# Kernel optimization log

Hardware: AMD Instinct MI355X
Metric: run time of the kernel (lower is better)

Reference implementation:

```python
import jax, jax.numpy as jnp
import numpy as np

B, S, D, DH = 4, 2048, 1024, 64


def setup_inputs() -> dict:
    key = jax.random.key(0)
    ks = jax.random.split(key, 7)
    x = jax.random.normal(ks[0], (B, S, D), dtype=jnp.float32)
    def w(k):
        return jax.random.normal(k, (D, DH), dtype=jnp.float32) / np.sqrt(D).astype(np.float32)
    return {
        'x': x,
        'w_q_u': w(ks[1]), 'w_k_u': w(ks[2]), 'w_v_u': w(ks[3]),
        'w_q_c': w(ks[4]), 'w_k_c': w(ks[5]), 'w_v_c': w(ks[6]),
    }


def reference(x, w_q_u, w_k_u, w_v_u, w_q_c, w_k_c, w_v_c):
    b, n, _ = x.shape
    scale = w_q_u.shape[-1] ** -0.5
    # projections (LinearNoBias -> plain matmul)
    Q_u = x @ w_q_u
    K_u = x @ w_k_u
    V_u = x @ w_v_u
    Q_c = x @ w_q_c
    K_c = x @ w_k_c
    V_c = x @ w_v_c

    i = jnp.arange(n)
    causal = i[:, None] >= i[None, :]        # True where j <= i (binary causal / keep for S_c)
    lookahead = i[:, None] < i[None, :]      # True where j > i (allowed in sigmoid term)

    # term1: [b, n, n], zeroed above the diagonal via binary causal mask
    term1 = jnp.einsum('bid,bjd->bij', Q_c, V_u) * scale * causal.astype(x.dtype)

    # sigmoid gate: lookahead mask adds -inf on/below the diagonal -> sigmoid = 0 there
    logits_u = jnp.einsum('bid,bjd->bij', Q_u, K_u) * scale
    sigmoid_term = jax.nn.sigmoid(jnp.where(lookahead, logits_u, -jnp.inf))

    # nested n^3 matmul: S_u[b,i,k] = sum_j term1[b,i,j] * sigmoid_term[b,k,j]
    S_u = jnp.einsum('bij,bkj->bik', term1, sigmoid_term)

    S_c = jnp.where(causal, jnp.einsum('bid,bjd->bij', Q_c, K_c) * scale, -jnp.inf)

    attn = jax.nn.softmax(S_c - jax.nn.silu(S_u), axis=-1)
    return jnp.einsum('bij,bjd->bid', attn, V_c)
```

## Files before the change

### kernel.cpp

```cpp
#include <hip/hip_runtime.h>
#include <hip/hip_bf16.h>

typedef short bf16x8 __attribute__((ext_vector_type(8)));
typedef float f32x4  __attribute__((ext_vector_type(4)));
typedef _Float16 f16x4 __attribute__((ext_vector_type(4)));
typedef _Float16 f16x8 __attribute__((ext_vector_type(8)));

#define MFMA16(a,b,c)  __builtin_amdgcn_mfma_f32_16x16x32_bf16((a),(b),(c),0,0,0)
#define MFMAF16(a,b,c) __builtin_amdgcn_mfma_f32_16x16x32_f16((a),(b),(c),0,0,0)

#define GLDS16(g,l) __builtin_amdgcn_global_load_lds( \
    (const __attribute__((address_space(1))) void*)(g), \
    (__attribute__((address_space(3))) void*)(l), 16, 0, 0)

__device__ __forceinline__ short f2bf(float f){
  union { float f; unsigned u; } v; v.f = f;
  unsigned r = v.u + 0x7fffu + ((v.u >> 16) & 1u);
  return (short)(r >> 16);
}
__device__ __forceinline__ float bf2f(short h){
  union { unsigned u; float f; } v; v.u = ((unsigned)(unsigned short)h) << 16;
  return v.f;
}
__device__ __forceinline__ void split8v(f32x4 a, f32x4 b, bf16x8& h, bf16x8& l){
  float t[8] = {a[0],a[1],a[2],a[3],b[0],b[1],b[2],b[3]};
  #pragma unroll
  for (int e = 0; e < 8; ++e){
    short hs = f2bf(t[e]);
    h[e] = hs;
    l[e] = f2bf(t[e] - bf2f(hs));
  }
}

__global__ void k_wt(const float* w0, const float* w1, const float* w2,
                     const float* w3, const float* w4, const float* w5,
                     unsigned short* __restrict__ wth, unsigned short* __restrict__ wtl){
  int p = blockIdx.y;
  const float* wp = p==0?w0:p==1?w1:p==2?w2:p==3?w3:p==4?w4:w5;
  int idx = blockIdx.x*256 + threadIdx.x;
  int n = idx >> 10, k = idx & 1023;
  float v = wp[k*64 + n];
  short hs = f2bf(v);
  wth[(size_t)p*65536 + n*1024 + k] = (unsigned short)hs;
  wtl[(size_t)p*65536 + n*1024 + k] = (unsigned short)f2bf(v - bf2f(hs));
}

__global__ void k_xsplit(const float* __restrict__ x,
                         unsigned short* __restrict__ xh, unsigned short* __restrict__ xl){
  size_t i = ((size_t)blockIdx.x*256 + threadIdx.x)*8;
  f32x4 a = *(const f32x4*)(x + i);
  f32x4 b = *(const f32x4*)(x + i + 4);
  bf16x8 h, l;
  split8v(a, b, h, l);
  *(bf16x8*)(xh + i) = h;
  *(bf16x8*)(xl + i) = l;
}

__global__ __launch_bounds__(256) void k_proj(
    const unsigned short* __restrict__ xh, const unsigned short* __restrict__ xl,
    const unsigned short* __restrict__ wth, const unsigned short* __restrict__ wtl,
    float* __restrict__ proj,
    unsigned short* __restrict__ projh, unsigned short* __restrict__ projl){
  __shared__ __align__(16) char sm[49152];
  int blk = blockIdx.x;
  int rb = blk/6, p = blk - rb*6;
  int tid = threadIdx.x, w = tid >> 6, lane = tid & 63;
  int lm = lane & 15, quad = lane >> 4;
  int srow = lane >> 3, scg = (lane & 7) ^ srow;
  const char* xhg = (const char*)xh;
  const char* xlg = (const char*)xl;
  const char* wthp = (const char*)wth + (size_t)p*131072;
  const char* wtlp = (const char*)wtl + (size_t)p*131072;
  int wm = w*32;
  f32x4 acc[2][4] = {};
  for (int k0 = 0; k0 < 1024; k0 += 64){
    __syncthreads();
    size_t cb = (size_t)k0*2 + scg*16;
    #pragma unroll
    for (int i2 = 0; i2 < 4; ++i2){
      int i = w*4 + i2;
      size_t g = (size_t)(rb*128 + i*8 + srow)*2048 + cb;
      GLDS16(xhg + g, sm +         i*1024);
      GLDS16(xlg + g, sm + 16384 + i*1024);
    }
    #pragma unroll
    for (int i2 = 0; i2 < 2; ++i2){
      int i = w*2 + i2;
      size_t g = (size_t)(i*8 + srow)*2048 + cb;
      GLDS16(wthp + g, sm + 32768 + i*1024);
      GLDS16(wtlp + g, sm + 40960 + i*1024);
    }
    __syncthreads();
    #pragma unroll
    for (int ks = 0; ks < 2; ++ks){
      bf16x8 bh[4], bl[4];
      #pragma unroll
      for (int n = 0; n < 4; ++n){
        int r = n*16 + lm;
        int off = r*128 + (((ks*4+quad) ^ (r&7))*16);
        bh[n] = *(const bf16x8*)(sm + 32768 + off);
        bl[n] = *(const bf16x8*)(sm + 40960 + off);
      }
      #pragma unroll
      for (int m = 0; m < 2; ++m){
        int r = wm + m*16 + lm;
        int off = r*128 + (((ks*4+quad) ^ (r&7))*16);
        bf16x8 ah = *(const bf16x8*)(sm + off);
        bf16x8 al = *(const bf16x8*)(sm + 16384 + off);
        #pragma unroll
        for (int n = 0; n < 4; ++n){
          acc[m][n] = MFMA16(ah, bh[n], acc[m][n]);
          acc[m][n] = MFMA16(ah, bl[n], acc[m][n]);
          acc[m][n] = MFMA16(al, bh[n], acc[m][n]);
        }
      }
    }
  }
  if (p == 5){
    float* op = proj + (size_t)p*524288;
    #pragma unroll
    for (int m = 0; m < 2; ++m)
      #pragma unroll
      for (int n = 0; n < 4; ++n)
        #pragma unroll
        for (int e = 0; e < 4; ++e){
          int r = rb*128 + wm + m*16 + quad*4 + e;
          op[(size_t)r*64 + n*16 + lm] = acc[m][n][e];
        }
  } else {
    unsigned short* oph = projh + (size_t)p*524288;
    unsigned short* opl = projl + (size_t)p*524288;
    #pragma unroll
    for (int m = 0; m < 2; ++m)
      #pragma unroll
      for (int n = 0; n < 4; ++n)
        #pragma unroll
        for (int e = 0; e < 4; ++e){
          int r = rb*128 + wm + m*16 + quad*4 + e;
          float f = acc[m][n][e];
          short hs = f2bf(f);
          oph[(size_t)r*64 + n*16 + lm] = (unsigned short)hs;
          opl[(size_t)r*64 + n*16 + lm] = (unsigned short)f2bf(f - bf2f(hs));
        }
  }
}

__global__ void k_vct(const float* __restrict__ proj, _Float16* __restrict__ vct){
  __shared__ float T[64][65];
  int b = blockIdx.y, st = blockIdx.x;
  int tid = threadIdx.x;
  const float* vc = proj + 5*524288 + (size_t)b*131072;
  int sloc = tid >> 2, cp = (tid & 3)*16;
  #pragma unroll
  for (int j = 0; j < 4; ++j){
    f32x4 v = *(const f32x4*)(vc + (size_t)(st*64 + sloc)*64 + cp + j*4);
    #pragma unroll
    for (int e = 0; e < 4; ++e) T[sloc][cp + j*4 + e] = v[e];
  }
  __syncthreads();
  int d = tid >> 2, sp = (tid & 3)*16;
  f16x8 h0, h1;
  #pragma unroll
  for (int j = 0; j < 8; ++j) h0[j] = (_Float16)T[sp + j][d];
  #pragma unroll
  for (int j = 0; j < 8; ++j) h1[j] = (_Float16)T[sp + 8 + j][d];
  size_t o = (size_t)b*131072 + (size_t)d*2048 + st*64 + sp;
  *(f16x8*)(vct + o) = h0; *(f16x8*)(vct + o + 8) = h1;
}

__global__ __launch_bounds__(256,2) void k_p2(
    const unsigned short* __restrict__ ph, const unsigned short* __restrict__ pl,
    _Float16* __restrict__ t1, _Float16* __restrict__ sg){
  __shared__ __align__(16) char sm[65536];
  int b = blockIdx.y;
  int t = blockIdx.x;
  bool isSig = t >= 136;
  if (isSig) t -= 136;
  int a = 0, bb = 0;
  #pragma unroll 1
  for (int aa = 0; aa < 16; ++aa){
    int c = isSig ? (16 - aa) : (aa + 1);
    if (t < c){ a = aa; bb = isSig ? (aa + t) : t; break; }
    t -= c;
  }
  int pa = isSig ? 0 : 3;
  int pb = isSig ? 1 : 2;
  const char* Ahg = (const char*)ph + (size_t)pa*1048576;
  const char* Alg = (const char*)pl + (size_t)pa*1048576;
  const char* Bhg = (const char*)ph + (size_t)pb*1048576;
  const char* Blg = (const char*)pl + (size_t)pb*1048576;
  int tid = threadIdx.x, w = tid >> 6, lane = tid & 63;
  int lm = lane & 15, quad = lane >> 4;
  int srow = lane >> 3, scg = (lane & 7) ^ srow;
  int wm = (w & 1)*64, wn = (w >> 1)*64;
  #pragma unroll
  for (int i2 = 0; i2 < 4; ++i2){
    int i = w*4 + i2;
    int rl = i*8 + srow;
    size_t ga = (size_t)(b*2048 + a*128  + rl)*128 + scg*16;
    size_t gb = (size_t)(b*2048 + bb*128 + rl)*128 + scg*16;
    GLDS16(Ahg + ga, sm +         i*1024);
    GLDS16(Alg + ga, sm + 16384 + i*1024);
    GLDS16(Bhg + gb, sm + 32768 + i*1024);
    GLDS16(Blg + gb, sm + 49152 + i*1024);
  }
  __syncthreads();
  f32x4 acc[4][4] = {};
  #pragma unroll
  for (int ks = 0; ks < 2; ++ks){
    bf16x8 bh[4], bl[4];
    #pragma unroll
    for (int n = 0; n < 4; ++n){
      int r = wn + n*16 + lm;
      int off = r*128 + (((ks*4+quad) ^ (r&7))*16);
      bh[n] = *(const bf16x8*)(sm + 32768 + off);
      bl[n] = *(const bf16x8*)(sm + 49152 + off);
    }
    #pragma unroll
    for (int m = 0; m < 4; ++m){
      int r = wm + m*16 + lm;
      int off = r*128 + (((ks*4+quad) ^ (r&7))*16);
      bf16x8 ah = *(const bf16x8*)(sm + off);
      bf16x8 al = *(const bf16x8*)(sm + 16384 + off);
      #pragma unroll
      for (int n = 0; n < 4; ++n){
        acc[m][n] = MFMA16(ah, bh[n], acc[m][n]);
        acc[m][n] = MFMA16(ah, bl[n], acc[m][n]);
        acc[m][n] = MFMA16(al, bh[n], acc[m][n]);
      }
    }
  }
  __syncthreads();
  _Float16* Tt = (_Float16*)sm;
  #pragma unroll
  for (int m = 0; m < 4; ++m){
    #pragma unroll
    for (int n = 0; n < 4; ++n){
      #pragma unroll
      for (int e = 0; e < 4; ++e){
        int il = wm + m*16 + quad*4 + e;
        int jl = wn + n*16 + lm;
        int gi = a*128 + il, gj = bb*128 + jl;
        float v = acc[m][n][e] * 0.125f;
        float outv;
        if (!isSig) outv = (gj <= gi) ? v : 0.0f;
        else        outv = (gj >  gi) ? (1.0f/(1.0f + __expf(-v))) : 0.0f;
        Tt[il*128 + jl] = (_Float16)outv;
      }
    }
  }
  __syncthreads();
  _Float16* outp = (isSig ? sg : t1) + (size_t)b*4194304;
  #pragma unroll
  for (int r = 0; r < 8; ++r){
    int lrow = w*32 + r*4 + (lane >> 4);
    int c16 = lane & 15;
    f32x4 vv = *(const f32x4*)(sm + lrow*256 + c16*16);
    *(f32x4*)((char*)(outp + (size_t)(a*128 + lrow)*2048 + bb*128) + c16*16) = vv;
  }
}

__global__ __launch_bounds__(256,2) void k_p3(
    const unsigned short* __restrict__ ph, const unsigned short* __restrict__ pl,
    const _Float16* __restrict__ t1, const _Float16* __restrict__ sg,
    _Float16* __restrict__ lg){
  __shared__ __align__(16) char sm[32768];
  int b = blockIdx.y;
  int v = blockIdx.x, I = 0, K = 0;
  #pragma unroll 1
  for (int d = 15; d >= 0; --d){
    int nd = 16 - d;
    if (v < nd){ I = d + v; K = v; break; }
    v -= nd;
  }
  int tid = threadIdx.x, w = tid >> 6, lane = tid & 63;
  int lm = lane & 15, quad = lane >> 4;
  size_t mat = (size_t)b * 4194304;
  const char* Ag = (const char*)(t1 + mat);
  const char* Bg = (const char*)(sg + mat);
  int srow = lane >> 3, scg = (lane & 7) ^ srow;
  int wm = (w & 1)*64, wn = (w >> 1)*64;
  f32x4 su[4][4] = {};
  for (int j64 = 2*K; j64 <= 2*I + 1; ++j64){
    __syncthreads();
    size_t colb = (size_t)j64*128 + scg*16;
    #pragma unroll
    for (int i2 = 0; i2 < 4; ++i2){
      int i = w*4 + i2;
      int rl = i*8 + srow;
      GLDS16(Ag + (size_t)(I*128 + rl)*4096 + colb, sm +         i*1024);
      GLDS16(Bg + (size_t)(K*128 + rl)*4096 + colb, sm + 16384 + i*1024);
    }
    __syncthreads();
    #pragma unroll
    for (int ks = 0; ks < 2; ++ks){
      f16x8 bf[4];
      #pragma unroll
      for (int n = 0; n < 4; ++n){
        int r = wn + n*16 + lm;
        bf[n] = *(const f16x8*)(sm + 16384 + r*128 + (((ks*4+quad) ^ (r&7))*16));
      }
      #pragma unroll
      for (int m = 0; m < 4; ++m){
        int r = wm + m*16 + lm;
        f16x8 af = *(const f16x8*)(sm + r*128 + (((ks*4+quad) ^ (r&7))*16));
        #pragma unroll
        for (int n = 0; n < 4; ++n)
          su[m][n] = MFMAF16(af, bf[n], su[m][n]);
      }
    }
  }
  const char* Qh = (const char*)ph + (size_t)3*1048576;
  const char* Ql = (const char*)pl + (size_t)3*1048576;
  const char* Kh = (const char*)ph + (size_t)4*1048576;
  const char* Kl = (const char*)pl + (size_t)4*1048576;
  f32x4 sc[4][4] = {};
  #pragma unroll
  for (int ks = 0; ks < 2; ++ks){
    bf16x8 kh[4], kl[4];
    #pragma unroll
    for (int n = 0; n < 4; ++n){
      size_t off = (size_t)(b*2048 + K*128 + wn + n*16 + lm)*128 + (ks*32 + quad*8)*2;
      kh[n] = *(const bf16x8*)(Kh + off);
      kl[n] = *(const bf16x8*)(Kl + off);
    }
    #pragma unroll
    for (int m = 0; m < 4; ++m){
      size_t off = (size_t)(b*2048 + I*128 + wm + m*16 + lm)*128 + (ks*32 + quad*8)*2;
      bf16x8 ah = *(const bf16x8*)(Qh + off);
      bf16x8 al = *(const bf16x8*)(Ql + off);
      #pragma unroll
      for (int n = 0; n < 4; ++n){
        sc[m][n] = MFMA16(ah, kh[n], sc[m][n]);
        sc[m][n] = MFMA16(ah, kl[n], sc[m][n]);
        sc[m][n] = MFMA16(al, kh[n], sc[m][n]);
      }
    }
  }
  __syncthreads();
  _Float16* Tt = (_Float16*)sm;
  #pragma unroll
  for (int m = 0; m < 4; ++m){
    #pragma unroll
    for (int n = 0; n < 4; ++n){
      #pragma unroll
      for (int e = 0; e < 4; ++e){
        int il = wm + m*16 + quad*4 + e;
        int jl = wn + n*16 + lm;
        float xv = su[m][n][e];
        float sgm = 1.0f/(1.0f + __expf(-xv));
        Tt[il*128 + jl] = (_Float16)(sc[m][n][e]*0.125f - xv*sgm);
      }
    }
  }
  __syncthreads();
  _Float16* lgb = lg + mat;
  #pragma unroll
  for (int r = 0; r < 8; ++r){
    int lrow = w*32 + r*4 + (lane >> 4);
    int c16 = lane & 15;
    f32x4 vv = *(const f32x4*)(sm + lrow*256 + c16*16);
    *(f32x4*)((char*)(lgb + (size_t)(I*128 + lrow)*2048 + K*128) + c16*16) = vv;
  }
}

__global__ __launch_bounds__(256) void k_p4a(const _Float16* __restrict__ lg,
    float* __restrict__ mrow, float* __restrict__ zrow){
  int b = blockIdx.y;
  int wid = blockIdx.x*4 + (threadIdx.x >> 6);
  int row = 2047 - wid;
  int lane = threadIdx.x & 63;
  const _Float16* lr = lg + (size_t)b*4194304u + (size_t)row*2048;
  float m_r = -1.0e30f, s_r = 0.0f;
  int nch = (row >> 9) + 1;
  for (int it = 0; it < nch; ++it){
    int base = it*512 + lane*8;
    if (base <= row){
      f16x8 vv = *(const f16x8*)(lr + base);
      float xs[8]; float mc = -1.0e30f;
      #pragma unroll
      for (int e = 0; e < 8; ++e){
        xs[e] = (base + e <= row) ? (float)vv[e] : -1.0e30f;
        mc = fmaxf(mc, xs[e]);
      }
      float mm = fmaxf(m_r, mc);
      float s = 0.0f;
      #pragma unroll
      for (int e = 0; e < 8; ++e)
        if (xs[e] > -1.0e29f) s += __expf(xs[e] - mm);
      s_r = (m_r > -1.0e29f ? s_r*__expf(m_r - mm) : 0.0f) + s;
      m_r = mm;
    }
  }
  #pragma unroll
  for (int off = 32; off; off >>= 1){
    float mo = __shfl_xor(m_r, off);
    float so = __shfl_xor(s_r, off);
    float mm = fmaxf(m_r, mo);
    float s = 0.0f;
    if (m_r > -1.0e29f) s += s_r*__expf(m_r - mm);
    if (mo  > -1.0e29f) s += so *__expf(mo  - mm);
    m_r = mm; s_r = s;
  }
  if (lane == 0){
    mrow[b*2048 + row] = m_r;
    zrow[b*2048 + row] = s_r;
  }
}

__global__ __launch_bounds__(256) void k_p4b(const _Float16* __restrict__ lg,
    const _Float16* __restrict__ vct,
    const float* __restrict__ mrow, const float* __restrict__ zrow,
    float* __restrict__ out){
  __shared__ __align__(16) float Ot[4][16][64];
  __shared__ __align__(16) _Float16 Ls[4][16][64];
  int b = blockIdx.y;
  int band = 127 - blockIdx.x;
  int r0 = band*16;
  int tid = threadIdx.x, w = tid >> 6, lane = tid & 63;
  int lm = lane & 15, quad = lane >> 4;
  const _Float16* lgb = lg + (size_t)b*4194304u;
  const _Float16* vb = vct + (size_t)b*131072;
  int arow = r0 + lm;
  float mv = mrow[b*2048 + arow];
  int nkt = ((r0 + 15) >> 6) + 1;
  int fc = (r0 + 1) >> 6;
  int sr = lane >> 2, sc4 = (lane & 3)*16;
  f32x4 acc[4] = {};
  for (int kt = w; kt < nkt; kt += 4){
    const _Float16* src = lgb + (size_t)(r0 + sr)*2048 + kt*64 + sc4;
    *(f16x8*)&Ls[w][sr][sc4]     = *(const f16x8*)src;
    *(f16x8*)&Ls[w][sr][sc4 + 8] = *(const f16x8*)(src + 8);
    bool full = kt < fc;
    #pragma unroll
    for (int ks = 0; ks < 2; ++ks){
      int jbase = kt*64 + ks*32 + quad*8;
      f16x8 Lv = *(const f16x8*)&Ls[w][lm][ks*32 + quad*8];
      f16x8 af;
      #pragma unroll
      for (int e = 0; e < 8; ++e){
        float p = __expf((float)Lv[e] - mv);
        if (!full && (jbase + e > arow)) p = 0.0f;
        af[e] = (_Float16)p;
      }
      #pragma unroll
      for (int n = 0; n < 4; ++n){
        f16x8 bv = *(const f16x8*)(vb + (size_t)(n*16 + lm)*2048 + jbase);
        acc[n] = MFMAF16(af, bv, acc[n]);
      }
    }
  }
  #pragma unroll
  for (int n = 0; n < 4; ++n)
    #pragma unroll
    for (int e = 0; e < 4; ++e)
      Ot[w][quad*4 + e][n*16 + lm] = acc[n][e];
  __syncthreads();
  int row = tid >> 4, c4 = (tid & 15)*4;
  f32x4 s = *(const f32x4*)&Ot[0][row][c4];
  #pragma unroll
  for (int ww = 1; ww < 4; ++ww){
    f32x4 t = *(const f32x4*)&Ot[ww][row][c4];
    s[0]+=t[0]; s[1]+=t[1]; s[2]+=t[2]; s[3]+=t[3];
  }
  float z = zrow[b*2048 + r0 + row];
  f32x4 o = { s[0]/z, s[1]/z, s[2]/z, s[3]/z };
  *(f32x4*)(out + ((size_t)b*2048 + r0 + row)*64 + c4) = o;
}

static const size_t OFF_PROJ  = 0;
static const size_t OFF_WTH   = 12582912;
static const size_t OFF_WTL   = 13369344;
static const size_t OFF_PROJH = 14155776;
static const size_t OFF_PROJL = 20447232;
static const size_t OFF_VCT   = 26738688;
static const size_t OFF_T1    = 27787264;
static const size_t OFF_SG    = 61341696;
static const size_t OFF_LG    = 94896128;
static const size_t OFF_XH    = 128450560;
static const size_t OFF_XL    = 145227776;

extern "C" void kernel_launch(void* const* d_in, const int* in_sizes, int n_in,
                              void* d_out, int out_size, void* d_ws, size_t ws_size,
                              hipStream_t stream){
  (void)in_sizes; (void)n_in; (void)out_size; (void)ws_size;
  const float* x = (const float*)d_in[0];
  char* ws = (char*)d_ws;
  float*          proj  = (float*)(ws + OFF_PROJ);
  unsigned short* wth   = (unsigned short*)(ws + OFF_WTH);
  unsigned short* wtl   = (unsigned short*)(ws + OFF_WTL);
  unsigned short* projh = (unsigned short*)(ws + OFF_PROJH);
  unsigned short* projl = (unsigned short*)(ws + OFF_PROJL);
  _Float16*       vct   = (_Float16*)(ws + OFF_VCT);
  _Float16*       t1    = (_Float16*)(ws + OFF_T1);
  _Float16*       sg    = (_Float16*)(ws + OFF_SG);
  _Float16*       lg    = (_Float16*)(ws + OFF_LG);
  unsigned short* xh    = (unsigned short*)(ws + OFF_XH);
  unsigned short* xl    = (unsigned short*)(ws + OFF_XL);
  float*          mbuf  = (float*)(ws + OFF_WTH);
  float*          zbuf  = (float*)(ws + OFF_WTL);

  k_wt    <<<dim3(256,6),  256, 0, stream>>>((const float*)d_in[1], (const float*)d_in[2],
                                             (const float*)d_in[3], (const float*)d_in[4],
                                             (const float*)d_in[5], (const float*)d_in[6], wth, wtl);
  k_xsplit<<<dim3(4096),   256, 0, stream>>>(x, xh, xl);
  k_proj  <<<dim3(384),    256, 0, stream>>>(xh, xl, wth, wtl, proj, projh, projl);
  k_vct   <<<dim3(32,4),   256, 0, stream>>>(proj, vct);
  k_p2    <<<dim3(272,4),  256, 0, stream>>>(projh, projl, t1, sg);
  k_p3    <<<dim3(136,4),  256, 0, stream>>>(projh, projl, t1, sg, lg);
  k_p4a   <<<dim3(512,4),  256, 0, stream>>>(lg, mbuf, zbuf);
  k_p4b   <<<dim3(128,4),  256, 0, stream>>>(lg, vct, mbuf, zbuf, (float*)d_out);
}
```

Baseline: 227.9 us.

## Retile projection, double-buffer p3 loads, fuse softmax stats into PV kernel

Three separate changes. The projection kernel now tiles 64 rows by two weight matrices per block instead of 128 rows by one, so x is reloaded fewer times across outputs. The nested-matmul kernel double-buffers its LDS tiles (64KB), overlapping global-to-LDS loads with MFMA work. The separate row max/sum kernel is merged into the PV kernel: each block loads its 16-row band of logits into LDS once, computes max and sum there, then reuses it for the weighted sum, removing one launch and one read of the logits. The cost is larger LDS per block, which may limit occupancy, and extra syncthreads.

```diff
diff --git a/kernel.cpp b/kernel.cpp
--- a/kernel.cpp
+++ b/kernel.cpp
@@ -3,7 +3,6 @@
 
 typedef short bf16x8 __attribute__((ext_vector_type(8)));
 typedef float f32x4  __attribute__((ext_vector_type(4)));
-typedef _Float16 f16x4 __attribute__((ext_vector_type(4)));
 typedef _Float16 f16x8 __attribute__((ext_vector_type(8)));
 
 #define MFMA16(a,b,c)  __builtin_amdgcn_mfma_f32_16x16x32_bf16((a),(b),(c),0,0,0)
@@ -63,85 +62,80 @@
     unsigned short* __restrict__ projh, unsigned short* __restrict__ projl){
   __shared__ __align__(16) char sm[49152];
   int blk = blockIdx.x;
-  int rb = blk/6, p = blk - rb*6;
+  int rb = blk/3, pg = blk - rb*3;
   int tid = threadIdx.x, w = tid >> 6, lane = tid & 63;
   int lm = lane & 15, quad = lane >> 4;
   int srow = lane >> 3, scg = (lane & 7) ^ srow;
   const char* xhg = (const char*)xh;
   const char* xlg = (const char*)xl;
-  const char* wthp = (const char*)wth + (size_t)p*131072;
-  const char* wtlp = (const char*)wtl + (size_t)p*131072;
-  int wm = w*32;
+  const char* w0h = (const char*)wth + (size_t)(pg*2  )*131072;
+  const char* w0l = (const char*)wtl + (size_t)(pg*2  )*131072;
+  const char* w1h = (const char*)wth + (size_t)(pg*2+1)*131072;
+  const char* w1l = (const char*)wtl + (size_t)(pg*2+1)*131072;
   f32x4 acc[2][4] = {};
   for (int k0 = 0; k0 < 1024; k0 += 64){
     __syncthreads();
     size_t cb = (size_t)k0*2 + scg*16;
     #pragma unroll
-    for (int i2 = 0; i2 < 4; ++i2){
-      int i = w*4 + i2;
-      size_t g = (size_t)(rb*128 + i*8 + srow)*2048 + cb;
-      GLDS16(xhg + g, sm +         i*1024);
-      GLDS16(xlg + g, sm + 16384 + i*1024);
-    }
-    #pragma unroll
     for (int i2 = 0; i2 < 2; ++i2){
       int i = w*2 + i2;
-      size_t g = (size_t)(i*8 + srow)*2048 + cb;
-      GLDS16(wthp + g, sm + 32768 + i*1024);
-      GLDS16(wtlp + g, sm + 40960 + i*1024);
+      size_t gx = (size_t)(rb*64 + i*8 + srow)*2048 + cb;
+      size_t gw = (size_t)(i*8 + srow)*2048 + cb;
+      GLDS16(xhg + gx, sm +         i*1024);
+      GLDS16(xlg + gx, sm +  8192 + i*1024);
+      GLDS16(w0h + gw, sm + 16384 + i*1024);
+      GLDS16(w0l + gw, sm + 24576 + i*1024);
+      GLDS16(w1h + gw, sm + 32768 + i*1024);
+      GLDS16(w1l + gw, sm + 40960 + i*1024);
     }
     __syncthreads();
     #pragma unroll
     for (int ks = 0; ks < 2; ++ks){
-      bf16x8 bh[4], bl[4];
-      #pragma unroll
-      for (int n = 0; n < 4; ++n){
-        int r = n*16 + lm;
-        int off = r*128 + (((ks*4+quad) ^ (r&7))*16);
-        bh[n] = *(const bf16x8*)(sm + 32768 + off);
-        bl[n] = *(const bf16x8*)(sm + 40960 + off);
-      }
-      #pragma unroll
-      for (int m = 0; m < 2; ++m){
-        int r = wm + m*16 + lm;
-        int off = r*128 + (((ks*4+quad) ^ (r&7))*16);
-        bf16x8 ah = *(const bf16x8*)(sm + off);
-        bf16x8 al = *(const bf16x8*)(sm + 16384 + off);
+      int ra = w*16 + lm;
+      int offa = ra*128 + (((ks*4+quad) ^ (ra&7))*16);
+      bf16x8 ah = *(const bf16x8*)(sm + offa);
+      bf16x8 al = *(const bf16x8*)(sm + 8192 + offa);
+      #pragma unroll
+      for (int sub = 0; sub < 2; ++sub){
         #pragma unroll
         for (int n = 0; n < 4; ++n){
-          acc[m][n] = MFMA16(ah, bh[n], acc[m][n]);
-          acc[m][n] = MFMA16(ah, bl[n], acc[m][n]);
-          acc[m][n] = MFMA16(al, bh[n], acc[m][n]);
+          int r = n*16 + lm;
+          int off = r*128 + (((ks*4+quad) ^ (r&7))*16);
+          bf16x8 bh = *(const bf16x8*)(sm + 16384 + sub*16384 + off);
+          bf16x8 bl = *(const bf16x8*)(sm + 24576 + sub*16384 + off);
+          acc[sub][n] = MFMA16(ah, bh, acc[sub][n]);
+          acc[sub][n] = MFMA16(ah, bl, acc[sub][n]);
+          acc[sub][n] = MFMA16(al, bh, acc[sub][n]);
         }
       }
     }
   }
-  if (p == 5){
-    float* op = proj + (size_t)p*524288;
-    #pragma unroll
-    for (int m = 0; m < 2; ++m)
+  #pragma unroll
+  for (int sub = 0; sub < 2; ++sub){
+    int p = pg*2 + sub;
+    if (p == 5){
+      float* op = proj + (size_t)5*524288;
       #pragma unroll
       for (int n = 0; n < 4; ++n)
         #pragma unroll
         for (int e = 0; e < 4; ++e){
-          int r = rb*128 + wm + m*16 + quad*4 + e;
-          op[(size_t)r*64 + n*16 + lm] = acc[m][n][e];
+          int r = rb*64 + w*16 + quad*4 + e;
+          op[(size_t)r*64 + n*16 + lm] = acc[sub][n][e];
         }
-  } else {
-    unsigned short* oph = projh + (size_t)p*524288;
-    unsigned short* opl = projl + (size_t)p*524288;
-    #pragma unroll
-    for (int m = 0; m < 2; ++m)
+    } else {
+      unsigned short* oph = projh + (size_t)p*524288;
+      unsigned short* opl = projl + (size_t)p*524288;
       #pragma unroll
       for (int n = 0; n < 4; ++n)
         #pragma unroll
         for (int e = 0; e < 4; ++e){
-          int r = rb*128 + wm + m*16 + quad*4 + e;
-          float f = acc[m][n][e];
+          int r = rb*64 + w*16 + quad*4 + e;
+          float f = acc[sub][n][e];
           short hs = f2bf(f);
           oph[(size_t)r*64 + n*16 + lm] = (unsigned short)hs;
           opl[(size_t)r*64 + n*16 + lm] = (unsigned short)f2bf(f - bf2f(hs));
         }
+    }
   }
 }
 
@@ -264,7 +258,7 @@
     const unsigned short* __restrict__ ph, const unsigned short* __restrict__ pl,
     const _Float16* __restrict__ t1, const _Float16* __restrict__ sg,
     _Float16* __restrict__ lg){
-  __shared__ __align__(16) char sm[32768];
+  __shared__ __align__(16) char sm[65536];
   int b = blockIdx.y;
   int v = blockIdx.x, I = 0, K = 0;
   #pragma unroll 1
@@ -280,30 +274,38 @@
   const char* Bg = (const char*)(sg + mat);
   int srow = lane >> 3, scg = (lane & 7) ^ srow;
   int wm = (w & 1)*64, wn = (w >> 1)*64;
-  f32x4 su[4][4] = {};
-  for (int j64 = 2*K; j64 <= 2*I + 1; ++j64){
-    __syncthreads();
+  int nsteps = 2*(I - K) + 2;
+  int j0 = 2*K;
+
+  auto stage = [&](int j64, int base){
     size_t colb = (size_t)j64*128 + scg*16;
     #pragma unroll
     for (int i2 = 0; i2 < 4; ++i2){
       int i = w*4 + i2;
       int rl = i*8 + srow;
-      GLDS16(Ag + (size_t)(I*128 + rl)*4096 + colb, sm +         i*1024);
-      GLDS16(Bg + (size_t)(K*128 + rl)*4096 + colb, sm + 16384 + i*1024);
-    }
+      GLDS16(Ag + (size_t)(I*128 + rl)*4096 + colb, sm + base +         i*1024);
+      GLDS16(Bg + (size_t)(K*128 + rl)*4096 + colb, sm + base + 16384 + i*1024);
+    }
+  };
+
+  f32x4 su[4][4] = {};
+  stage(j0, 0);
+  for (int step = 0; step < nsteps; ++step){
+    int cur = (step & 1) << 15;
     __syncthreads();
+    if (step + 1 < nsteps) stage(j0 + step + 1, (~step & 1) << 15);
     #pragma unroll
     for (int ks = 0; ks < 2; ++ks){
       f16x8 bf[4];
       #pragma unroll
       for (int n = 0; n < 4; ++n){
         int r = wn + n*16 + lm;
-        bf[n] = *(const f16x8*)(sm + 16384 + r*128 + (((ks*4+quad) ^ (r&7))*16));
+        bf[n] = *(const f16x8*)(sm + cur + 16384 + r*128 + (((ks*4+quad) ^ (r&7))*16));
       }
       #pragma unroll
       for (int m = 0; m < 4; ++m){
         int r = wm + m*16 + lm;
-        f16x8 af = *(const f16x8*)(sm + r*128 + (((ks*4+quad) ^ (r&7))*16));
+        f16x8 af = *(const f16x8*)(sm + cur + r*128 + (((ks*4+quad) ^ (r&7))*16));
         #pragma unroll
         for (int n = 0; n < 4; ++n)
           su[m][n] = MFMAF16(af, bf[n], su[m][n]);
@@ -364,83 +366,74 @@
   }
 }
 
-__global__ __launch_bounds__(256) void k_p4a(const _Float16* __restrict__ lg,
-    float* __restrict__ mrow, float* __restrict__ zrow){
-  int b = blockIdx.y;
-  int wid = blockIdx.x*4 + (threadIdx.x >> 6);
-  int row = 2047 - wid;
-  int lane = threadIdx.x & 63;
-  const _Float16* lr = lg + (size_t)b*4194304u + (size_t)row*2048;
-  float m_r = -1.0e30f, s_r = 0.0f;
-  int nch = (row >> 9) + 1;
-  for (int it = 0; it < nch; ++it){
-    int base = it*512 + lane*8;
-    if (base <= row){
-      f16x8 vv = *(const f16x8*)(lr + base);
-      float xs[8]; float mc = -1.0e30f;
-      #pragma unroll
-      for (int e = 0; e < 8; ++e){
-        xs[e] = (base + e <= row) ? (float)vv[e] : -1.0e30f;
-        mc = fmaxf(mc, xs[e]);
-      }
-      float mm = fmaxf(m_r, mc);
-      float s = 0.0f;
-      #pragma unroll
-      for (int e = 0; e < 8; ++e)
-        if (xs[e] > -1.0e29f) s += __expf(xs[e] - mm);
-      s_r = (m_r > -1.0e29f ? s_r*__expf(m_r - mm) : 0.0f) + s;
-      m_r = mm;
-    }
-  }
-  #pragma unroll
-  for (int off = 32; off; off >>= 1){
-    float mo = __shfl_xor(m_r, off);
-    float so = __shfl_xor(s_r, off);
-    float mm = fmaxf(m_r, mo);
-    float s = 0.0f;
-    if (m_r > -1.0e29f) s += s_r*__expf(m_r - mm);
-    if (mo  > -1.0e29f) s += so *__expf(mo  - mm);
-    m_r = mm; s_r = s;
-  }
-  if (lane == 0){
-    mrow[b*2048 + row] = m_r;
-    zrow[b*2048 + row] = s_r;
-  }
-}
-
-__global__ __launch_bounds__(256) void k_p4b(const _Float16* __restrict__ lg,
-    const _Float16* __restrict__ vct,
-    const float* __restrict__ mrow, const float* __restrict__ zrow,
-    float* __restrict__ out){
-  __shared__ __align__(16) float Ot[4][16][64];
-  __shared__ __align__(16) _Float16 Ls[4][16][64];
+__global__ __launch_bounds__(256,2) void k_p4(const _Float16* __restrict__ lg,
+    const _Float16* __restrict__ vct, float* __restrict__ out){
+  __shared__ __align__(16) char sm[66048];
+  float* Mz = (float*)(sm + 65536);
+  float* Sz = (float*)(sm + 65792);
   int b = blockIdx.y;
   int band = 127 - blockIdx.x;
   int r0 = band*16;
   int tid = threadIdx.x, w = tid >> 6, lane = tid & 63;
   int lm = lane & 15, quad = lane >> 4;
-  const _Float16* lgb = lg + (size_t)b*4194304u;
+  const char* lgb = (const char*)lg + ((size_t)b*4194304 + (size_t)r0*2048)*2;
   const _Float16* vb = vct + (size_t)b*131072;
-  int arow = r0 + lm;
-  float mv = mrow[b*2048 + arow];
   int nkt = ((r0 + 15) >> 6) + 1;
   int fc = (r0 + 1) >> 6;
-  int sr = lane >> 2, sc4 = (lane & 3)*16;
+  int srl = lane >> 3, ssl = lane & 7;
+  for (int kt = w; kt < nkt; kt += 4){
+    #pragma unroll
+    for (int i2 = 0; i2 < 2; ++i2){
+      int rl = i2*8 + srl;
+      GLDS16(lgb + (size_t)rl*4096 + kt*128 + ((ssl ^ (rl & 7))*16),
+             sm + kt*2048 + i2*1024);
+    }
+  }
+  __syncthreads();
+  float m_r = -3.0e38f;
+  for (int kt = w; kt < nkt; kt += 4){
+    #pragma unroll
+    for (int half = 0; half < 2; ++half){
+      int sl = quad*2 + half;
+      f16x8 v = *(const f16x8*)(sm + kt*2048 + lm*128 + ((sl ^ (lm & 7))*16));
+      int cb = kt*64 + sl*8;
+      #pragma unroll
+      for (int e = 0; e < 8; ++e)
+        m_r = (cb + e <= r0 + lm) ? fmaxf(m_r, (float)v[e]) : m_r;
+    }
+  }
+  m_r = fmaxf(m_r, __shfl_xor(m_r, 16));
+  m_r = fmaxf(m_r, __shfl_xor(m_r, 32));
+  Mz[w*16 + lm] = m_r;
+  __syncthreads();
+  float mfin = fmaxf(fmaxf(Mz[lm], Mz[16 + lm]), fmaxf(Mz[32 + lm], Mz[48 + lm]));
+  float s_r = 0.0f;
+  for (int kt = w; kt < nkt; kt += 4){
+    #pragma unroll
+    for (int half = 0; half < 2; ++half){
+      int sl = quad*2 + half;
+      f16x8 v = *(const f16x8*)(sm + kt*2048 + lm*128 + ((sl ^ (lm & 7))*16));
+      int cb = kt*64 + sl*8;
+      #pragma unroll
+      for (int e = 0; e < 8; ++e)
+        if (cb + e <= r0 + lm) s_r += __expf((float)v[e] - mfin);
+    }
+  }
+  s_r += __shfl_xor(s_r, 16);
+  s_r += __shfl_xor(s_r, 32);
+  Sz[w*16 + lm] = s_r;
   f32x4 acc[4] = {};
   for (int kt = w; kt < nkt; kt += 4){
-    const _Float16* src = lgb + (size_t)(r0 + sr)*2048 + kt*64 + sc4;
-    *(f16x8*)&Ls[w][sr][sc4]     = *(const f16x8*)src;
-    *(f16x8*)&Ls[w][sr][sc4 + 8] = *(const f16x8*)(src + 8);
     bool full = kt < fc;
     #pragma unroll
     for (int ks = 0; ks < 2; ++ks){
+      f16x8 Lv = *(const f16x8*)(sm + kt*2048 + lm*128 + (((ks*4+quad) ^ (lm & 7))*16));
       int jbase = kt*64 + ks*32 + quad*8;
-      f16x8 Lv = *(const f16x8*)&Ls[w][lm][ks*32 + quad*8];
       f16x8 af;
       #pragma unroll
       for (int e = 0; e < 8; ++e){
-        float p = __expf((float)Lv[e] - mv);
-        if (!full && (jbase + e > arow)) p = 0.0f;
+        float p = __expf((float)Lv[e] - mfin);
+        if (!full && (jbase + e > r0 + lm)) p = 0.0f;
         af[e] = (_Float16)p;
       }
       #pragma unroll
@@ -450,20 +443,22 @@
       }
     }
   }
+  __syncthreads();
+  float* Ot = (float*)sm;
   #pragma unroll
   for (int n = 0; n < 4; ++n)
     #pragma unroll
     for (int e = 0; e < 4; ++e)
-      Ot[w][quad*4 + e][n*16 + lm] = acc[n][e];
+      Ot[(w*16 + quad*4 + e)*64 + n*16 + lm] = acc[n][e];
   __syncthreads();
   int row = tid >> 4, c4 = (tid & 15)*4;
-  f32x4 s = *(const f32x4*)&Ot[0][row][c4];
+  f32x4 s = *(const f32x4*)&Ot[row*64 + c4];
   #pragma unroll
   for (int ww = 1; ww < 4; ++ww){
-    f32x4 t = *(const f32x4*)&Ot[ww][row][c4];
-    s[0]+=t[0]; s[1]+=t[1]; s[2]+=t[2]; s[3]+=t[3];
-  }
-  float z = zrow[b*2048 + r0 + row];
+    f32x4 t2 = *(const f32x4*)&Ot[(ww*16 + row)*64 + c4];
+    s[0]+=t2[0]; s[1]+=t2[1]; s[2]+=t2[2]; s[3]+=t2[3];
+  }
+  float z = Sz[row] + Sz[16 + row] + Sz[32 + row] + Sz[48 + row];
   f32x4 o = { s[0]/z, s[1]/z, s[2]/z, s[3]/z };
   *(f32x4*)(out + ((size_t)b*2048 + r0 + row)*64 + c4) = o;
 }
@@ -497,8 +492,6 @@
   _Float16*       lg    = (_Float16*)(ws + OFF_LG);
   unsigned short* xh    = (unsigned short*)(ws + OFF_XH);
   unsigned short* xl    = (unsigned short*)(ws + OFF_XL);
-  float*          mbuf  = (float*)(ws + OFF_WTH);
-  float*          zbuf  = (float*)(ws + OFF_WTL);
 
   k_wt    <<<dim3(256,6),  256, 0, stream>>>((const float*)d_in[1], (const float*)d_in[2],
                                              (const float*)d_in[3], (const float*)d_in[4],
@@ -508,6 +501,5 @@
   k_vct   <<<dim3(32,4),   256, 0, stream>>>(proj, vct);
   k_p2    <<<dim3(272,4),  256, 0, stream>>>(projh, projl, t1, sg);
   k_p3    <<<dim3(136,4),  256, 0, stream>>>(projh, projl, t1, sg, lg);
-  k_p4a   <<<dim3(512,4),  256, 0, stream>>>(lg, mbuf, zbuf);
-  k_p4b   <<<dim3(128,4),  256, 0, stream>>>(lg, vct, mbuf, zbuf, (float*)d_out);
-}
+  k_p4    <<<dim3(128,4),  256, 0, stream>>>(lg, vct, (float*)d_out);
+}
```

Result: faster. 218.6 us (-4.1%).
